# Performance work log

Hardware: AMD Instinct MI355X
Metric: run time of the kernel (lower is better)

The kernel has to match this reference:

```python
import jax, jax.numpy as jnp
import numpy as np

NUM_EXPERTS = 8
TOP_K = 2
N_EMBD = 1024
D_FFN = 2048  # 4*n_embd // top_k, already block-aligned


def setup_inputs() -> dict:
    key = jax.random.key(0)
    k1, k2, k3, k4 = jax.random.split(key, 4)
    x = jax.random.normal(k1, (4, 2048, N_EMBD), jnp.float32)
    w_router = jax.random.normal(k2, (N_EMBD, NUM_EXPERTS), jnp.float32) * 0.02
    w1 = jax.random.normal(k3, (N_EMBD, D_FFN * NUM_EXPERTS), jnp.float32) * 0.02
    w2 = jax.random.normal(k4, (D_FFN * NUM_EXPERTS, N_EMBD), jnp.float32) * 0.02
    return {"x": x, "w_router": w_router, "w1": w1, "w2": w2}


def reference(x, w_router, w1, w2):
    B, S, D = x.shape
    T = B * S
    xf = x.reshape(T, D)

    # --- routing ---
    logits = xf @ w_router                                   # [T, E]
    probs = jax.nn.softmax(logits.astype(jnp.float32), axis=-1)
    topw, topi = jax.lax.top_k(probs, TOP_K)                 # [T, K]
    topw = topw / topw.sum(-1, keepdims=True)                # norm_topk_prob
    topw = topw.astype(x.dtype)

    # dense combine weights [T, E]: router weight where selected, else 0
    wd = jnp.zeros((T, NUM_EXPERTS), x.dtype)
    wd = wd.at[jnp.arange(T)[:, None], topi].add(topw)

    # --- grouped (per-expert) GEMM; source has NO nonlinearity between w1/w2 ---
    w1r = w1.reshape(D, NUM_EXPERTS, D_FFN)   # column layout is expert-major
    w2r = w2.reshape(NUM_EXPERTS, D_FFN, D)
    out = jnp.zeros((T, D), x.dtype)
    for e in range(NUM_EXPERTS):
        h = xf @ w1r[:, e, :]                 # [T, F]
        out = out + wd[:, e:e+1] * (h @ w2r[e])
    out = out.reshape(B, S, D)

    # --- aux losses ---
    router_z_loss = jnp.mean(
        jax.scipy.special.logsumexp(logits.astype(jnp.float32), axis=-1) ** 2)
    p_i = probs.mean(axis=0)                                  # [E]
    f_i = jnp.zeros(NUM_EXPERTS, x.dtype).at[topi.reshape(-1)].add(
        jnp.asarray(1.0 / (T * TOP_K), x.dtype))
    load_balance_loss = NUM_EXPERTS * (f_i @ p_i.astype(x.dtype))
    return out, router_z_loss, load_balance_loss, f_i
```

## Files before the change

kernel.cpp:

```cpp
#include <hip/hip_runtime.h>
#include <hip/hip_bf16.h>
#include <stdint.h>
#include <stddef.h>


typedef unsigned short ushort_t;
typedef __attribute__((ext_vector_type(8))) short short8;
typedef __attribute__((ext_vector_type(4))) float floatx4;

#define T_TOK 8192
#define NE    8
#define DD    1024
#define FF    2048
#define W1ROW (NE * FF)

#define BM 128
#define BN 128
#define BK 64

__device__ __forceinline__ unsigned short f2bf(float f) {
  union { float f; unsigned u; } c; c.f = f;
  unsigned r = c.u + 0x7fffu + ((c.u >> 16) & 1u);
  return (unsigned short)(r >> 16);
}
__device__ __forceinline__ unsigned packbf2(float a, float b) {
  unsigned ua = __float_as_uint(a) + 0x8000u;
  unsigned ub = __float_as_uint(b) + 0x8000u;
  return __builtin_amdgcn_perm(ub, ua, 0x07060302);
}

static const size_t OFF_CNT   = 0;
static const size_t OFF_ZPART = 256;
static const size_t OFF_PPART = 512;
static const size_t OFF_REXP  = 4096;
static const size_t OFF_RWTS  = 36864;
static const size_t OFF_IDS   = 102400;
static const size_t OFF_WTS   = 364544;
static const size_t OFF_W2T   = 1048576;
static const size_t OFF_MT    = OFF_W2T + 33554432;

__global__ __launch_bounds__(256)
void router_kernel(const float* __restrict__ x, const float* __restrict__ wrt,
                   unsigned* __restrict__ rexp, float2* __restrict__ rwts,
                   float* __restrict__ zpart, float* __restrict__ ppart) {
  int w = threadIdx.x >> 6, ln = threadIdx.x & 63;
  int t = blockIdx.x * 4 + w;
  const float* xr = x + (size_t)t * DD;
  float acc[8] = {0.f, 0.f, 0.f, 0.f, 0.f, 0.f, 0.f, 0.f};
  for (int i = 0; i < 16; ++i) {
    int d = ln + (i << 6);
    float xv = xr[d];
    float4 r0 = *(const float4*)(wrt + (size_t)d * 8);
    float4 r1 = *(const float4*)(wrt + (size_t)d * 8 + 4);
    acc[0] += xv * r0.x;  acc[1] += xv * r0.y;
    acc[2] += xv * r0.z;  acc[3] += xv * r0.w;
    acc[4] += xv * r1.x;  acc[5] += xv * r1.y;
    acc[6] += xv * r1.z;  acc[7] += xv * r1.w;
  }
#pragma unroll
  for (int e = 0; e < 8; ++e) {
#pragma unroll
    for (int off = 32; off > 0; off >>= 1) acc[e] += __shfl_xor(acc[e], off, 64);
  }
  if (ln == 0) {
    float m = acc[0];
#pragma unroll
    for (int e = 1; e < 8; ++e) m = fmaxf(m, acc[e]);
    float p[8], s = 0.f;
#pragma unroll
    for (int e = 0; e < 8; ++e) { p[e] = expf(acc[e] - m); s += p[e]; }
    float z = m + logf(s);
    int e1 = 0; float v1 = acc[0];
#pragma unroll
    for (int e = 1; e < 8; ++e) if (acc[e] > v1) { v1 = acc[e]; e1 = e; }
    int e2 = (e1 == 0) ? 1 : 0; float v2 = acc[e2];
#pragma unroll
    for (int e = 0; e < 8; ++e) if (e != e1 && acc[e] > v2) { v2 = acc[e]; e2 = e; }
    float p1 = p[e1], p2 = p[e2];
    float inv = 1.f / (p1 + p2);
    rexp[t] = (unsigned)e1 | ((unsigned)e2 << 8);
    rwts[t] = make_float2(p1 * inv, p2 * inv);
    int sh = blockIdx.x & 63;
    unsafeAtomicAdd(&zpart[sh], z * z);
    float sinv = 1.f / s;
#pragma unroll
    for (int e = 0; e < 8; ++e) unsafeAtomicAdd(&ppart[sh * 8 + e], p[e] * sinv);
  }
}

__global__ __launch_bounds__(256)
void build_lists_kernel(const unsigned* __restrict__ rexp, const float2* __restrict__ rwts,
                        int* __restrict__ cnt, int* __restrict__ ids, float* __restrict__ wts) {
  __shared__ int lcnt[8];
  __shared__ int lbase[8];
  if (threadIdx.x < 8) lcnt[threadIdx.x] = 0;
  __syncthreads();
  int t = blockIdx.x * 256 + threadIdx.x;
  unsigned re = rexp[t];
  float2 w = rwts[t];
  int e1 = (int)(re & 0xffu), e2 = (int)((re >> 8) & 0xffu);
  int p1 = atomicAdd(&lcnt[e1], 1);
  int p2 = atomicAdd(&lcnt[e2], 1);
  __syncthreads();
  if (threadIdx.x < 8) lbase[threadIdx.x] = atomicAdd(&cnt[threadIdx.x], lcnt[threadIdx.x]);
  __syncthreads();
  int i1 = e1 * T_TOK + lbase[e1] + p1;
  ids[i1] = t;  wts[i1] = w.x;
  int i2 = e2 * T_TOK + lbase[e2] + p2;
  ids[i2] = t;  wts[i2] = w.y;
}

__global__ __launch_bounds__(256)
void transpose_w2_kernel(const float* __restrict__ w2, ushort_t* __restrict__ W2T) {
  __shared__ ushort_t tile[64 * 72];
  int e = blockIdx.z, f0 = blockIdx.x * 64, j0 = blockIdx.y * 64;
  int tid = (int)threadIdx.x;
  int r = tid >> 2, c0 = (tid & 3) * 16;
  const float* src = w2 + ((size_t)(e * FF + f0 + r)) * DD + j0 + c0;
  float4 v0 = *(const float4*)(src);
  float4 v1 = *(const float4*)(src + 4);
  float4 v2 = *(const float4*)(src + 8);
  float4 v3 = *(const float4*)(src + 12);
  uint4 pa = make_uint4(packbf2(v0.x, v0.y), packbf2(v0.z, v0.w),
                        packbf2(v1.x, v1.y), packbf2(v1.z, v1.w));
  uint4 pb = make_uint4(packbf2(v2.x, v2.y), packbf2(v2.z, v2.w),
                        packbf2(v3.x, v3.y), packbf2(v3.z, v3.w));
  *(uint4*)&tile[r * 72 + c0]     = pa;
  *(uint4*)&tile[r * 72 + c0 + 8] = pb;
  __syncthreads();
  int j = tid >> 2, g0 = (tid & 3) * 16;
  ushort_t o[16];
#pragma unroll
  for (int i = 0; i < 16; ++i) o[i] = tile[(g0 + i) * 72 + j];
  ushort_t* dst = W2T + ((size_t)(e * DD + j0 + j)) * FF + f0 + g0;
  *(uint4*)(dst)     = *(uint4*)&o[0];
  *(uint4*)(dst + 8) = *(uint4*)&o[8];
}

__global__ __launch_bounds__(256)
void gemm_mt_kernel(const ushort_t* __restrict__ W2T, const float* __restrict__ w1,
                    ushort_t* __restrict__ MT) {
  int e = blockIdx.z;
  int n0 = blockIdx.x * BN;
  int m0 = blockIdx.y * BM;
  __shared__ alignas(16) ushort_t As[BM * BK];
  __shared__ alignas(16) ushort_t Bs[BN * BK];
  const ushort_t* Abase = W2T + (size_t)e * DD * FF;
  int tid = (int)threadIdx.x;
  int w = tid >> 6, ln = tid & 63;
  int wr = w >> 1, wc = w & 1;
  int mrow = ln & 15, kq = ln >> 4;
  floatx4 acc[4][4] = {};
  for (int k0 = 0; k0 < FF; k0 += BK) {
    __syncthreads();
#pragma unroll
    for (int it = 0; it < 4; ++it) {
      int c = it * 256 + tid;
      int r = c >> 3, b = c & 7;
      uint4 v = *(const uint4*)(Abase + (size_t)(m0 + r) * FF + k0 + b * 8);
      *(uint4*)&As[r * BK + ((b ^ (r & 7)) << 3)] = v;
    }
#pragma unroll
    for (int it = 0; it < 4; ++it) {
      int c = it * 256 + tid;
      int r = c >> 3, b = c & 7;
      const float* p = w1 + (size_t)(n0 + r) * W1ROW + e * FF + k0 + b * 8;
      float4 f0 = *(const float4*)(p);
      float4 f1 = *(const float4*)(p + 4);
      uint4 pk = make_uint4(packbf2(f0.x, f0.y), packbf2(f0.z, f0.w),
                            packbf2(f1.x, f1.y), packbf2(f1.z, f1.w));
      *(uint4*)&Bs[r * BK + ((b ^ (r & 7)) << 3)] = pk;
    }
    __syncthreads();
#pragma unroll
    for (int s = 0; s < 2; ++s) {
      short8 fa[4], fb[4];
#pragma unroll
      for (int i = 0; i < 4; ++i) {
        int r = wr * 64 + i * 16 + mrow;
        fa[i] = *(const short8*)&As[r * BK + ((((s << 2) | kq) ^ (r & 7)) << 3)];
      }
#pragma unroll
      for (int j = 0; j < 4; ++j) {
        int r = wc * 64 + j * 16 + mrow;
        fb[j] = *(const short8*)&Bs[r * BK + ((((s << 2) | kq) ^ (r & 7)) << 3)];
      }
#pragma unroll
      for (int i = 0; i < 4; ++i)
#pragma unroll
        for (int j = 0; j < 4; ++j)
          acc[i][j] = __builtin_amdgcn_mfma_f32_16x16x32_bf16(fa[i], fb[j], acc[i][j], 0, 0, 0);
    }
  }
  ushort_t* outp = MT + (size_t)e * DD * DD;
#pragma unroll
  for (int i = 0; i < 4; ++i) {
#pragma unroll
    for (int j = 0; j < 4; ++j) {
#pragma unroll
      for (int rr = 0; rr < 4; ++rr) {
        int m = m0 + wr * 64 + i * 16 + kq * 4 + rr;
        int n = n0 + wc * 64 + j * 16 + mrow;
        outp[(size_t)m * DD + n] = f2bf(acc[i][j][rr]);
      }
    }
  }
}

__global__ __launch_bounds__(256)
void gemm_moe_kernel(const float* __restrict__ x, const ushort_t* __restrict__ MT,
                     const int* __restrict__ cnt, const int* __restrict__ ids,
                     const float* __restrict__ wts, float* __restrict__ outp) {
  int e = blockIdx.z;
  int ce = cnt[e];
  int s0 = blockIdx.y * BM;
  if (s0 >= ce) return;
  int n0 = blockIdx.x * BN;
  __shared__ int   rid_l[BM];
  __shared__ float wrow[BM];
  __shared__ alignas(16) ushort_t As[BM * BK];
  __shared__ alignas(16) ushort_t Bs[BN * BK];
  int tid = (int)threadIdx.x;
  if (tid < BM) {
    int s = s0 + tid;
    if (s < ce) { rid_l[tid] = ids[e * T_TOK + s]; wrow[tid] = wts[e * T_TOK + s]; }
    else        { rid_l[tid] = 0;                  wrow[tid] = 0.f; }
  }
  __syncthreads();
  const ushort_t* Bbase = MT + (size_t)e * DD * DD;
  int w = tid >> 6, ln = tid & 63;
  int wr = w >> 1, wc = w & 1;
  int mrow = ln & 15, kq = ln >> 4;
  floatx4 acc[4][4] = {};
  for (int k0 = 0; k0 < DD; k0 += BK) {
    __syncthreads();
#pragma unroll
    for (int it = 0; it < 4; ++it) {
      int c = it * 256 + tid;
      int r = c >> 3, b = c & 7;
      int tok = rid_l[r];
      const float* p = x + (size_t)tok * DD + k0 + b * 8;
      float4 f0 = *(const float4*)(p);
      float4 f1 = *(const float4*)(p + 4);
      uint4 pk = make_uint4(packbf2(f0.x, f0.y), packbf2(f0.z, f0.w),
                            packbf2(f1.x, f1.y), packbf2(f1.z, f1.w));
      *(uint4*)&As[r * BK + ((b ^ (r & 7)) << 3)] = pk;
    }
#pragma unroll
    for (int it = 0; it < 4; ++it) {
      int c = it * 256 + tid;
      int r = c >> 3, b = c & 7;
      uint4 v = *(const uint4*)(Bbase + (size_t)(n0 + r) * DD + k0 + b * 8);
      *(uint4*)&Bs[r * BK + ((b ^ (r & 7)) << 3)] = v;
    }
    __syncthreads();
#pragma unroll
    for (int s = 0; s < 2; ++s) {
      short8 fa[4], fb[4];
#pragma unroll
      for (int i = 0; i < 4; ++i) {
        int r = wr * 64 + i * 16 + mrow;
        fa[i] = *(const short8*)&As[r * BK + ((((s << 2) | kq) ^ (r & 7)) << 3)];
      }
#pragma unroll
      for (int j = 0; j < 4; ++j) {
        int r = wc * 64 + j * 16 + mrow;
        fb[j] = *(const short8*)&Bs[r * BK + ((((s << 2) | kq) ^ (r & 7)) << 3)];
      }
#pragma unroll
      for (int i = 0; i < 4; ++i)
#pragma unroll
        for (int j = 0; j < 4; ++j)
          acc[i][j] = __builtin_amdgcn_mfma_f32_16x16x32_bf16(fa[i], fb[j], acc[i][j], 0, 0, 0);
    }
  }
#pragma unroll
  for (int i = 0; i < 4; ++i) {
#pragma unroll
    for (int j = 0; j < 4; ++j) {
#pragma unroll
      for (int rr = 0; rr < 4; ++rr) {
        int mloc = wr * 64 + i * 16 + kq * 4 + rr;
        if (s0 + mloc < ce) {
          int tok = rid_l[mloc];
          int ncol = n0 + wc * 64 + j * 16 + mrow;
          unsafeAtomicAdd(&outp[(size_t)tok * DD + ncol], acc[i][j][rr] * wrow[mloc]);
        }
      }
    }
  }
}

__global__ void losses_kernel(const float* __restrict__ zpart, const float* __restrict__ ppart,
                              const int* __restrict__ cnt, float* __restrict__ outaux) {
  if (threadIdx.x == 0) {
    float z = 0.f;
    for (int i = 0; i < 64; ++i) z += zpart[i];
    z /= (float)T_TOK;
    float p[8];
    for (int e = 0; e < 8; ++e) {
      float s = 0.f;
      for (int b = 0; b < 64; ++b) s += ppart[b * 8 + e];
      p[e] = s / (float)T_TOK;
    }
    float lb = 0.f;
    for (int e = 0; e < 8; ++e) lb += ((float)cnt[e] / (float)(T_TOK * 2)) * p[e];
    lb *= (float)NE;
    outaux[0] = z;
    outaux[1] = lb;
    for (int e = 0; e < 8; ++e) outaux[2 + e] = (float)cnt[e] / (float)(T_TOK * 2);
  }
}

extern "C" void kernel_launch(void* const* d_in, const int* in_sizes, int n_in,
                              void* d_out, int out_size, void* d_ws, size_t ws_size,
                              hipStream_t stream) {
  const float* x   = (const float*)d_in[0];
  const float* wrt = (const float*)d_in[1];
  const float* w1  = (const float*)d_in[2];
  const float* w2  = (const float*)d_in[3];
  float* out = (float*)d_out;

  char* ws = (char*)d_ws;
  int*      cnt   = (int*)     (ws + OFF_CNT);
  float*    zpart = (float*)   (ws + OFF_ZPART);
  float*    ppart = (float*)   (ws + OFF_PPART);
  unsigned* rexp  = (unsigned*)(ws + OFF_REXP);
  float2*   rwts  = (float2*)  (ws + OFF_RWTS);
  int*      ids   = (int*)     (ws + OFF_IDS);
  float*    wtsf  = (float*)   (ws + OFF_WTS);
  ushort_t* W2T   = (ushort_t*)(ws + OFF_W2T);
  ushort_t* MT    = (ushort_t*)(ws + OFF_MT);

  hipMemsetAsync(d_ws, 0, 4096, stream);
  hipMemsetAsync(d_out, 0, (size_t)out_size * 4, stream);
  router_kernel<<<T_TOK / 4, 256, 0, stream>>>(x, wrt, rexp, rwts, zpart, ppart);
  build_lists_kernel<<<T_TOK / 256, 256, 0, stream>>>(rexp, rwts, cnt, ids, wtsf);
  transpose_w2_kernel<<<dim3(FF / 64, DD / 64, NE), 256, 0, stream>>>(w2, W2T);
  gemm_mt_kernel<<<dim3(DD / BN, DD / BM, NE), 256, 0, stream>>>(W2T, w1, MT);
  gemm_moe_kernel<<<dim3(DD / BN, T_TOK / BM, NE), 256, 0, stream>>>(x, MT, cnt, ids, wtsf, out);
  losses_kernel<<<1, 64, 0, stream>>>(zpart, ppart, cnt, out + (size_t)T_TOK * DD);
}
```

Before: 433.4 us.

## Pre-convert x to bf16 and use direct global-to-LDS loads in GEMMs

Adds a kernel that converts x to bf16 once into workspace (reusing the W2T region after the MT GEMM finishes). Both GEMMs then stage tiles with global_load_lds 16-byte loads, using precomputed swizzled pointers, instead of going through registers. The grid order is also changed so the expert index varies fastest, which affects scheduling and L2 reuse. The aim is to cut per-tile fp32 loads, conversion work and register staging. In exchange it adds an extra pass over x and a write of the bf16 copy.

```diff
diff --git a/kernel.cpp b/kernel.cpp
--- a/kernel.cpp
+++ b/kernel.cpp
@@ -17,6 +17,11 @@
 #define BM 128
 #define BN 128
 #define BK 64
+
+typedef const __attribute__((address_space(1))) unsigned int gas_u32;
+typedef __attribute__((address_space(3)))       unsigned int las_u32;
+#define GLOAD16(gp, lp) \
+  __builtin_amdgcn_global_load_lds((gas_u32*)(gp), (las_u32*)(lp), 16, 0, 0)
 
 __device__ __forceinline__ unsigned short f2bf(float f) {
   union { float f; unsigned u; } c; c.f = f;
@@ -38,6 +43,7 @@
 static const size_t OFF_WTS   = 364544;
 static const size_t OFF_W2T   = 1048576;
 static const size_t OFF_MT    = OFF_W2T + 33554432;
+static const size_t OFF_XB    = OFF_W2T;
 
 __global__ __launch_bounds__(256)
 void router_kernel(const float* __restrict__ x, const float* __restrict__ wrt,
@@ -138,11 +144,21 @@
 }
 
 __global__ __launch_bounds__(256)
+void convert_x_kernel(const float* __restrict__ x, ushort_t* __restrict__ XB) {
+  size_t i = ((size_t)blockIdx.x * 256 + threadIdx.x) * 8;
+  float4 f0 = *(const float4*)(x + i);
+  float4 f1 = *(const float4*)(x + i + 4);
+  uint4 pk = make_uint4(packbf2(f0.x, f0.y), packbf2(f0.z, f0.w),
+                        packbf2(f1.x, f1.y), packbf2(f1.z, f1.w));
+  *(uint4*)(XB + i) = pk;
+}
+
+__global__ __launch_bounds__(256)
 void gemm_mt_kernel(const ushort_t* __restrict__ W2T, const float* __restrict__ w1,
                     ushort_t* __restrict__ MT) {
-  int e = blockIdx.z;
-  int n0 = blockIdx.x * BN;
+  int e  = blockIdx.x;
   int m0 = blockIdx.y * BM;
+  int n0 = blockIdx.z * BN;
   __shared__ alignas(16) ushort_t As[BM * BK];
   __shared__ alignas(16) ushort_t Bs[BN * BK];
   const ushort_t* Abase = W2T + (size_t)e * DD * FF;
@@ -150,16 +166,19 @@
   int w = tid >> 6, ln = tid & 63;
   int wr = w >> 1, wc = w & 1;
   int mrow = ln & 15, kq = ln >> 4;
+  const ushort_t* agp[4];
+#pragma unroll
+  for (int it = 0; it < 4; ++it) {
+    int r  = w * 32 + it * 8 + (ln >> 3);
+    int cs = (ln & 7) ^ (r & 7);
+    agp[it] = Abase + (size_t)(m0 + r) * FF + cs * 8;
+  }
   floatx4 acc[4][4] = {};
   for (int k0 = 0; k0 < FF; k0 += BK) {
     __syncthreads();
 #pragma unroll
-    for (int it = 0; it < 4; ++it) {
-      int c = it * 256 + tid;
-      int r = c >> 3, b = c & 7;
-      uint4 v = *(const uint4*)(Abase + (size_t)(m0 + r) * FF + k0 + b * 8);
-      *(uint4*)&As[r * BK + ((b ^ (r & 7)) << 3)] = v;
-    }
+    for (int it = 0; it < 4; ++it)
+      GLOAD16(agp[it] + k0, &As[(w * 32 + it * 8) * BK]);
 #pragma unroll
     for (int it = 0; it < 4; ++it) {
       int c = it * 256 + tid;
@@ -208,14 +227,14 @@
 }
 
 __global__ __launch_bounds__(256)
-void gemm_moe_kernel(const float* __restrict__ x, const ushort_t* __restrict__ MT,
+void gemm_moe_kernel(const ushort_t* __restrict__ XB, const ushort_t* __restrict__ MT,
                      const int* __restrict__ cnt, const int* __restrict__ ids,
                      const float* __restrict__ wts, float* __restrict__ outp) {
-  int e = blockIdx.z;
+  int e = blockIdx.x;
   int ce = cnt[e];
   int s0 = blockIdx.y * BM;
   if (s0 >= ce) return;
-  int n0 = blockIdx.x * BN;
+  int n0 = blockIdx.z * BN;
   __shared__ int   rid_l[BM];
   __shared__ float wrow[BM];
   __shared__ alignas(16) ushort_t As[BM * BK];
@@ -231,28 +250,25 @@
   int w = tid >> 6, ln = tid & 63;
   int wr = w >> 1, wc = w & 1;
   int mrow = ln & 15, kq = ln >> 4;
+  const ushort_t* agp[4];
+  const ushort_t* bgp[4];
+#pragma unroll
+  for (int it = 0; it < 4; ++it) {
+    int r  = w * 32 + it * 8 + (ln >> 3);
+    int cs = (ln & 7) ^ (r & 7);
+    int tok = rid_l[r];
+    agp[it] = XB + (size_t)tok * DD + cs * 8;
+    bgp[it] = Bbase + (size_t)(n0 + r) * DD + cs * 8;
+  }
   floatx4 acc[4][4] = {};
   for (int k0 = 0; k0 < DD; k0 += BK) {
     __syncthreads();
 #pragma unroll
-    for (int it = 0; it < 4; ++it) {
-      int c = it * 256 + tid;
-      int r = c >> 3, b = c & 7;
-      int tok = rid_l[r];
-      const float* p = x + (size_t)tok * DD + k0 + b * 8;
-      float4 f0 = *(const float4*)(p);
-      float4 f1 = *(const float4*)(p + 4);
-      uint4 pk = make_uint4(packbf2(f0.x, f0.y), packbf2(f0.z, f0.w),
-                            packbf2(f1.x, f1.y), packbf2(f1.z, f1.w));
-      *(uint4*)&As[r * BK + ((b ^ (r & 7)) << 3)] = pk;
-    }
-#pragma unroll
-    for (int it = 0; it < 4; ++it) {
-      int c = it * 256 + tid;
-      int r = c >> 3, b = c & 7;
-      uint4 v = *(const uint4*)(Bbase + (size_t)(n0 + r) * DD + k0 + b * 8);
-      *(uint4*)&Bs[r * BK + ((b ^ (r & 7)) << 3)] = v;
-    }
+    for (int it = 0; it < 4; ++it)
+      GLOAD16(agp[it] + k0, &As[(w * 32 + it * 8) * BK]);
+#pragma unroll
+    for (int it = 0; it < 4; ++it)
+      GLOAD16(bgp[it] + k0, &Bs[(w * 32 + it * 8) * BK]);
     __syncthreads();
 #pragma unroll
     for (int s = 0; s < 2; ++s) {
@@ -331,13 +347,15 @@
   float*    wtsf  = (float*)   (ws + OFF_WTS);
   ushort_t* W2T   = (ushort_t*)(ws + OFF_W2T);
   ushort_t* MT    = (ushort_t*)(ws + OFF_MT);
+  ushort_t* XB    = (ushort_t*)(ws + OFF_XB);
 
   hipMemsetAsync(d_ws, 0, 4096, stream);
   hipMemsetAsync(d_out, 0, (size_t)out_size * 4, stream);
   router_kernel<<<T_TOK / 4, 256, 0, stream>>>(x, wrt, rexp, rwts, zpart, ppart);
   build_lists_kernel<<<T_TOK / 256, 256, 0, stream>>>(rexp, rwts, cnt, ids, wtsf);
   transpose_w2_kernel<<<dim3(FF / 64, DD / 64, NE), 256, 0, stream>>>(w2, W2T);
-  gemm_mt_kernel<<<dim3(DD / BN, DD / BM, NE), 256, 0, stream>>>(W2T, w1, MT);
-  gemm_moe_kernel<<<dim3(DD / BN, T_TOK / BM, NE), 256, 0, stream>>>(x, MT, cnt, ids, wtsf, out);
+  gemm_mt_kernel<<<dim3(NE, DD / BM, DD / BN), 256, 0, stream>>>(W2T, w1, MT);
+  convert_x_kernel<<<(T_TOK * DD) / (8 * 256), 256, 0, stream>>>(x, XB);
+  gemm_moe_kernel<<<dim3(NE, T_TOK / BM, DD / BN), 256, 0, stream>>>(XB, MT, cnt, ids, wtsf, out);
   losses_kernel<<<1, 64, 0, stream>>>(zpart, ppart, cnt, out + (size_t)T_TOK * DD);
 }
```

Measured after the change: 410.5 us. -5.3%, faster.
